# Performance work log

Measured on AMD Instinct MI355X. Metric: run time of the kernel, lower is better.

Reference implementation:

```python
import jax, jax.numpy as jnp
import numpy as np

BINS = 10
LOSS_WEIGHT = 1.0
EDGE_TOP = 1.0 + 1e-6  # edges[-1] += 1e-6 in the torch module


def setup_inputs() -> dict:
    key = jax.random.key(0)
    k1, k2, k3 = jax.random.split(key, 3)
    shape = (32, 1048576)
    # pred: sigmoid probabilities in [0, 1)
    pred = jax.random.uniform(k1, shape, dtype=jnp.float32)
    target = (jax.random.uniform(k2, shape) < 0.3).astype(jnp.float32)
    label_weight = (jax.random.uniform(k3, shape) < 0.95).astype(jnp.float32)
    return {"pred": pred, "target": target, "label_weight": label_weight}


def reference(pred, target, label_weight):
    p = pred.reshape(-1)
    t = target.reshape(-1).astype(p.dtype)
    lw = label_weight.reshape(-1).astype(p.dtype)

    I = jnp.sum(p * t)                       # intersection
    S = jnp.sum(p) + jnp.sum(t)              # denominator of Dice

    # gradient norm proxy: |2I/S * pred.detach() - target| (no grad flows through g)
    g = jax.lax.stop_gradient(jnp.abs(2.0 * I / S * p - t))

    valid = lw > 0
    tot = jnp.maximum(jnp.sum(valid.astype(p.dtype)), 1.0)

    # bin assignment: edges are i/bins for i=0..bins, with edges[-1] bumped by 1e-6,
    # so g in [i/bins, (i+1)/bins) -> bin i, and g in [1, 1+1e-6) -> bin bins-1.
    in_range = valid & (g < EDGE_TOP)
    bin_idx = jnp.clip(jnp.floor(g * BINS).astype(jnp.int32), 0, BINS - 1)

    # one-pass histogram of valid, in-range elements
    counts = jnp.zeros(BINS, dtype=p.dtype).at[bin_idx].add(in_range.astype(p.dtype))
    n_nonempty = jnp.sum(counts > 0).astype(p.dtype)

    # weight = tot / num_in_bin for elements in a non-empty bin, else 0; then /n
    per_elem = jnp.where(in_range, tot / jnp.maximum(counts[bin_idx], 1.0), 0.0)
    weights = per_elem / jnp.maximum(n_nonempty, 1.0)

    loss = 1.0 - jnp.sum(2.0 * p * t * weights) / S
    return loss * LOSS_WEIGHT
```

## Files before the change

### kernel.cpp

```cpp
#include <hip/hip_runtime.h>


constexpr int BINS = 10;
constexpr int K1   = 8;
constexpr int K2   = 8;
constexpr int CH1  = 256 * K1;
constexpr int CH2  = 256 * K2;
constexpr int OFF1 = 64;
constexpr int OFF2 = 16448;

__global__ __launch_bounds__(256) void k_reduce1(const float4* __restrict__ p,
                                                 const float4* __restrict__ t,
                                                 float* __restrict__ ws,
                                                 int n4, int n) {
    const int chunk = blockIdx.x * CH1;
    const int base  = chunk + threadIdx.x;
    float sI = 0.f, sP = 0.f, sT = 0.f;

    if (chunk + CH1 <= n4) {
        float4 pv[K1], tv[K1];
#pragma unroll
        for (int k = 0; k < K1; ++k) pv[k] = p[base + k * 256];
#pragma unroll
        for (int k = 0; k < K1; ++k) tv[k] = t[base + k * 256];
#pragma unroll
        for (int k = 0; k < K1; ++k) {
            sI += pv[k].x * tv[k].x + pv[k].y * tv[k].y + pv[k].z * tv[k].z + pv[k].w * tv[k].w;
            sP += pv[k].x + pv[k].y + pv[k].z + pv[k].w;
            sT += tv[k].x + tv[k].y + tv[k].z + tv[k].w;
        }
    } else {
        for (int k = 0; k < K1; ++k) {
            int i = base + k * 256;
            if (i < n4) {
                float4 pv = p[i], tv = t[i];
                sI += pv.x * tv.x + pv.y * tv.y + pv.z * tv.z + pv.w * tv.w;
                sP += pv.x + pv.y + pv.z + pv.w;
                sT += tv.x + tv.y + tv.z + tv.w;
            }
        }
    }
    if (blockIdx.x == 0 && threadIdx.x == 0) {
        const float* pf = (const float*)p;
        const float* tf = (const float*)t;
        for (int i = n4 * 4; i < n; ++i) { sI += pf[i] * tf[i]; sP += pf[i]; sT += tf[i]; }
    }
#pragma unroll
    for (int o = 32; o > 0; o >>= 1) {
        sI += __shfl_down(sI, o);
        sP += __shfl_down(sP, o);
        sT += __shfl_down(sT, o);
    }
    __shared__ float rI[4], rP[4], rT[4];
    int wave = threadIdx.x >> 6, lane = threadIdx.x & 63;
    if (lane == 0) { rI[wave] = sI; rP[wave] = sP; rT[wave] = sT; }
    __syncthreads();
    if (threadIdx.x == 0) {
        float* o = &ws[OFF1 + blockIdx.x * 4];
        o[0] = rI[0] + rI[1] + rI[2] + rI[3];
        o[1] = rP[0] + rP[1] + rP[2] + rP[3];
        o[2] = rT[0] + rT[1] + rT[2] + rT[3];
    }
}

__global__ __launch_bounds__(256) void k_mid(float* __restrict__ ws, int nb1) {
    const float4* pws = (const float4*)&ws[OFF1];
    float aI = 0.f, aP = 0.f, aT = 0.f;
    for (int b = threadIdx.x; b < nb1; b += 256) {
        float4 v = pws[b];
        aI += v.x; aP += v.y; aT += v.z;
    }
    __shared__ float red[256 * 5];
    float* mine = &red[threadIdx.x * 5];
    mine[0] = aI; mine[1] = aP; mine[2] = aT;
    __syncthreads();
    int tid = threadIdx.x;
    if (tid < 3) {
        float s = 0.f;
        for (int i = 0; i < 256; ++i) s += red[i * 5 + tid];
        red[tid] = s;
    }
    __syncthreads();
    if (tid == 0) {
        float I = red[0];
        float S = red[1] + red[2];
        ws[0] = 2.f * I / S;
        ws[1] = S;
    }
}

__global__ __launch_bounds__(256) void k_pass2(const float4* __restrict__ p,
                                               const float4* __restrict__ t,
                                               const float4* __restrict__ lw,
                                               float* __restrict__ ws,
                                               int n4, int n) {
    const float scale    = ws[0];
    const float edge_top = 1.0f + 1e-6f;

    float cnt[BINS], sm[BINS];
#pragma unroll
    for (int b = 0; b < BINS; ++b) { cnt[b] = 0.f; sm[b] = 0.f; }
    float vcount = 0.f;

    auto process = [&](float pe, float te, float we) {
        bool valid = we > 0.f;
        vcount += valid ? 1.f : 0.f;
        float g = fabsf(scale * pe - te);
        bool inr = valid && (g < edge_top);
        int b = (int)(g * 10.f);
        b = b > (BINS - 1) ? (BINS - 1) : b;
        float addc = inr ? 1.f : 0.f;
        float adds = inr ? 2.f * pe * te : 0.f;
#pragma unroll
        for (int b0 = 0; b0 < BINS; ++b0) {
            bool m = (b == b0);
            cnt[b0] += m ? addc : 0.f;
            sm[b0]  += m ? adds : 0.f;
        }
    };

    const int chunk = blockIdx.x * CH2;
    const int base  = chunk + threadIdx.x;

    if (chunk + CH2 <= n4) {
        float4 pv[K2], tv[K2], wv[K2];
#pragma unroll
        for (int k = 0; k < K2; ++k) pv[k] = p[base + k * 256];
#pragma unroll
        for (int k = 0; k < K2; ++k) tv[k] = t[base + k * 256];
#pragma unroll
        for (int k = 0; k < K2; ++k) wv[k] = lw[base + k * 256];
#pragma unroll
        for (int k = 0; k < K2; ++k) {
            process(pv[k].x, tv[k].x, wv[k].x);
            process(pv[k].y, tv[k].y, wv[k].y);
            process(pv[k].z, tv[k].z, wv[k].z);
            process(pv[k].w, tv[k].w, wv[k].w);
        }
    } else {
        for (int k = 0; k < K2; ++k) {
            int i = base + k * 256;
            if (i < n4) {
                float4 pv = p[i], tv = t[i], wv = lw[i];
                process(pv.x, tv.x, wv.x);
                process(pv.y, tv.y, wv.y);
                process(pv.z, tv.z, wv.z);
                process(pv.w, tv.w, wv.w);
            }
        }
    }
    if (blockIdx.x == 0 && threadIdx.x == 0) {
        const float* pf = (const float*)p;
        const float* tf = (const float*)t;
        const float* wf = (const float*)lw;
        for (int i = n4 * 4; i < n; ++i) process(pf[i], tf[i], wf[i]);
    }

    __shared__ float red[256 * 21];
    float* mine = &red[threadIdx.x * 21];
#pragma unroll
    for (int b0 = 0; b0 < BINS; ++b0) { mine[b0] = cnt[b0]; mine[BINS + b0] = sm[b0]; }
    mine[2 * BINS] = vcount;
    __syncthreads();

    int tid = threadIdx.x;
    if (tid < 2 * BINS + 1) {
        float v = 0.f;
        for (int i = 0; i < 256; ++i) v += red[i * 21 + tid];
        ws[OFF2 + blockIdx.x * 24 + tid] = v;
    }
}

__global__ __launch_bounds__(256) void k_final(const float* __restrict__ ws,
                                               float* __restrict__ out, int nb2) {
    float acc[24];
#pragma unroll
    for (int s = 0; s < 24; ++s) acc[s] = 0.f;

    for (int b = threadIdx.x; b < nb2; b += 256) {
        const float4* rec = (const float4*)&ws[OFF2 + b * 24];
        float4 v0 = rec[0], v1 = rec[1], v2 = rec[2],
               v3 = rec[3], v4 = rec[4], v5 = rec[5];
        acc[0]  += v0.x; acc[1]  += v0.y; acc[2]  += v0.z; acc[3]  += v0.w;
        acc[4]  += v1.x; acc[5]  += v1.y; acc[6]  += v1.z; acc[7]  += v1.w;
        acc[8]  += v2.x; acc[9]  += v2.y; acc[10] += v2.z; acc[11] += v2.w;
        acc[12] += v3.x; acc[13] += v3.y; acc[14] += v3.z; acc[15] += v3.w;
        acc[16] += v4.x; acc[17] += v4.y; acc[18] += v4.z; acc[19] += v4.w;
        acc[20] += v5.x;
    }

    __shared__ float red[256 * 25];
    float* mine = &red[threadIdx.x * 25];
#pragma unroll
    for (int s = 0; s <= 2 * BINS; ++s) mine[s] = acc[s];
    __syncthreads();

    __shared__ float fin[24];
    int tid = threadIdx.x;
    if (tid <= 2 * BINS) {
        float s = 0.f;
        for (int i = 0; i < 256; ++i) s += red[i * 25 + tid];
        fin[tid] = s;
    }
    __syncthreads();
    if (tid == 0) {
        float S   = ws[1];
        float tot = fmaxf(fin[20], 1.0f);
        int nne = 0;
        for (int b = 0; b < BINS; ++b) nne += (fin[b] > 0.f) ? 1 : 0;
        float nn = fmaxf((float)nne, 1.0f);
        float wsum = 0.f;
        for (int b = 0; b < BINS; ++b) {
            float c = fmaxf(fin[b], 1.0f);
            wsum += fin[BINS + b] * (tot / c);
        }
        wsum /= nn;
        out[0] = 1.0f - wsum / S;
    }
}

extern "C" void kernel_launch(void* const* d_in, const int* in_sizes, int n_in,
                              void* d_out, int out_size, void* d_ws, size_t ws_size,
                              hipStream_t stream) {
    const float* p  = (const float*)d_in[0];
    const float* t  = (const float*)d_in[1];
    const float* lw = (const float*)d_in[2];
    float* ws  = (float*)d_ws;
    float* out = (float*)d_out;
    int n  = in_sizes[0];
    int n4 = n >> 2;

    int nb1 = (n4 + CH1 - 1) / CH1;
    int nb2 = (n4 + CH2 - 1) / CH2;
    if (nb1 < 1) nb1 = 1;
    if (nb2 < 1) nb2 = 1;

    k_reduce1<<<nb1, 256, 0, stream>>>((const float4*)p, (const float4*)t, ws, n4, n);
    k_mid<<<1, 256, 0, stream>>>(ws, nb1);
    k_pass2<<<nb2, 256, 0, stream>>>((const float4*)p, (const float4*)t,
                                     (const float4*)lw, ws, n4, n);
    k_final<<<1, 256, 0, stream>>>(ws, out, nb2);
}
```

Measured before the change: 408.3 us.

## Use fixed-size grid-stride loops and integer bin counters in both reduction passes

```diff
diff --git a/kernel.cpp b/kernel.cpp
--- a/kernel.cpp
+++ b/kernel.cpp
@@ -1,49 +1,47 @@
 #include <hip/hip_runtime.h>
 
 
-constexpr int BINS = 10;
-constexpr int K1   = 8;
-constexpr int K2   = 8;
-constexpr int CH1  = 256 * K1;
-constexpr int CH2  = 256 * K2;
-constexpr int OFF1 = 64;
-constexpr int OFF2 = 16448;
+constexpr int BINS   = 10;
+constexpr int K      = 4;
+constexpr int CH     = 256 * K;
+constexpr int BLOCKS = 2048;
+constexpr int OFF1   = 64;
+constexpr int OFF2   = 16448;
 
 __global__ __launch_bounds__(256) void k_reduce1(const float4* __restrict__ p,
                                                  const float4* __restrict__ t,
                                                  float* __restrict__ ws,
                                                  int n4, int n) {
-    const int chunk = blockIdx.x * CH1;
-    const int base  = chunk + threadIdx.x;
+    const int tid   = threadIdx.x;
+    const int nfull = n4 / CH;
     float sI = 0.f, sP = 0.f, sT = 0.f;
 
-    if (chunk + CH1 <= n4) {
-        float4 pv[K1], tv[K1];
-#pragma unroll
-        for (int k = 0; k < K1; ++k) pv[k] = p[base + k * 256];
-#pragma unroll
-        for (int k = 0; k < K1; ++k) tv[k] = t[base + k * 256];
-#pragma unroll
-        for (int k = 0; k < K1; ++k) {
+    for (int c = blockIdx.x; c < nfull; c += gridDim.x) {
+        const int base = c * CH + tid;
+        float4 pv[K], tv[K];
+#pragma unroll
+        for (int k = 0; k < K; ++k) pv[k] = p[base + k * 256];
+#pragma unroll
+        for (int k = 0; k < K; ++k) tv[k] = t[base + k * 256];
+#pragma unroll
+        for (int k = 0; k < K; ++k) {
             sI += pv[k].x * tv[k].x + pv[k].y * tv[k].y + pv[k].z * tv[k].z + pv[k].w * tv[k].w;
             sP += pv[k].x + pv[k].y + pv[k].z + pv[k].w;
             sT += tv[k].x + tv[k].y + tv[k].z + tv[k].w;
         }
-    } else {
-        for (int k = 0; k < K1; ++k) {
-            int i = base + k * 256;
-            if (i < n4) {
-                float4 pv = p[i], tv = t[i];
-                sI += pv.x * tv.x + pv.y * tv.y + pv.z * tv.z + pv.w * tv.w;
-                sP += pv.x + pv.y + pv.z + pv.w;
-                sT += tv.x + tv.y + tv.z + tv.w;
-            }
-        }
-    }
-    if (blockIdx.x == 0 && threadIdx.x == 0) {
-        const float* pf = (const float*)p;
-        const float* tf = (const float*)t;
-        for (int i = n4 * 4; i < n; ++i) { sI += pf[i] * tf[i]; sP += pf[i]; sT += tf[i]; }
+    }
+    if (blockIdx.x == 0) {
+        for (int i = nfull * CH + tid; i < n4; i += 256) {
+            float4 pv = p[i], tv = t[i];
+            sI += pv.x * tv.x + pv.y * tv.y + pv.z * tv.z + pv.w * tv.w;
+            sP += pv.x + pv.y + pv.z + pv.w;
+            sT += tv.x + tv.y + tv.z + tv.w;
+        }
+        if (tid == 0) {
+            const float* pf = (const float*)p;
+            const float* tf = (const float*)t;
+            for (int i = n4 * 4; i < n; ++i) { sI += pf[i] * tf[i]; sP += pf[i]; sT += tf[i]; }
+        }
     }
 #pragma unroll
     for (int o = 32; o > 0; o >>= 1) {
@@ -52,10 +50,10 @@
         sT += __shfl_down(sT, o);
     }
     __shared__ float rI[4], rP[4], rT[4];
-    int wave = threadIdx.x >> 6, lane = threadIdx.x & 63;
+    int wave = tid >> 6, lane = tid & 63;
     if (lane == 0) { rI[wave] = sI; rP[wave] = sP; rT[wave] = sT; }
     __syncthreads();
-    if (threadIdx.x == 0) {
+    if (tid == 0) {
         float* o = &ws[OFF1 + blockIdx.x * 4];
         o[0] = rI[0] + rI[1] + rI[2] + rI[3];
         o[1] = rP[0] + rP[1] + rP[2] + rP[3];
@@ -96,74 +94,75 @@
                                                int n4, int n) {
     const float scale    = ws[0];
     const float edge_top = 1.0f + 1e-6f;
-
-    float cnt[BINS], sm[BINS];
-#pragma unroll
-    for (int b = 0; b < BINS; ++b) { cnt[b] = 0.f; sm[b] = 0.f; }
-    float vcount = 0.f;
+    const int tid   = threadIdx.x;
+    const int nfull = n4 / CH;
+
+    int   cnt[BINS];
+    float sm[BINS];
+#pragma unroll
+    for (int b = 0; b < BINS; ++b) { cnt[b] = 0; sm[b] = 0.f; }
+    int vcount = 0;
 
     auto process = [&](float pe, float te, float we) {
         bool valid = we > 0.f;
-        vcount += valid ? 1.f : 0.f;
+        vcount += valid;
         float g = fabsf(scale * pe - te);
         bool inr = valid && (g < edge_top);
         int b = (int)(g * 10.f);
         b = b > (BINS - 1) ? (BINS - 1) : b;
-        float addc = inr ? 1.f : 0.f;
-        float adds = inr ? 2.f * pe * te : 0.f;
+        int slot = inr ? b : BINS;
+        float adds = 2.f * pe * te;
 #pragma unroll
         for (int b0 = 0; b0 < BINS; ++b0) {
-            bool m = (b == b0);
-            cnt[b0] += m ? addc : 0.f;
+            bool m = (slot == b0);
+            cnt[b0] += m;
             sm[b0]  += m ? adds : 0.f;
         }
     };
 
-    const int chunk = blockIdx.x * CH2;
-    const int base  = chunk + threadIdx.x;
-
-    if (chunk + CH2 <= n4) {
-        float4 pv[K2], tv[K2], wv[K2];
-#pragma unroll
-        for (int k = 0; k < K2; ++k) pv[k] = p[base + k * 256];
-#pragma unroll
-        for (int k = 0; k < K2; ++k) tv[k] = t[base + k * 256];
-#pragma unroll
-        for (int k = 0; k < K2; ++k) wv[k] = lw[base + k * 256];
-#pragma unroll
-        for (int k = 0; k < K2; ++k) {
+    for (int c = blockIdx.x; c < nfull; c += gridDim.x) {
+        const int base = c * CH + tid;
+        float4 pv[K], tv[K], wv[K];
+#pragma unroll
+        for (int k = 0; k < K; ++k) pv[k] = p[base + k * 256];
+#pragma unroll
+        for (int k = 0; k < K; ++k) tv[k] = t[base + k * 256];
+#pragma unroll
+        for (int k = 0; k < K; ++k) wv[k] = lw[base + k * 256];
+#pragma unroll
+        for (int k = 0; k < K; ++k) {
             process(pv[k].x, tv[k].x, wv[k].x);
             process(pv[k].y, tv[k].y, wv[k].y);
             process(pv[k].z, tv[k].z, wv[k].z);
             process(pv[k].w, tv[k].w, wv[k].w);
         }
-    } else {
-        for (int k = 0; k < K2; ++k) {
-            int i = base + k * 256;
-            if (i < n4) {
-                float4 pv = p[i], tv = t[i], wv = lw[i];
-                process(pv.x, tv.x, wv.x);
-                process(pv.y, tv.y, wv.y);
-                process(pv.z, tv.z, wv.z);
-                process(pv.w, tv.w, wv.w);
-            }
-        }
-    }
-    if (blockIdx.x == 0 && threadIdx.x == 0) {
-        const float* pf = (const float*)p;
-        const float* tf = (const float*)t;
-        const float* wf = (const float*)lw;
-        for (int i = n4 * 4; i < n; ++i) process(pf[i], tf[i], wf[i]);
+    }
+    if (blockIdx.x == 0) {
+        for (int i = nfull * CH + tid; i < n4; i += 256) {
+            float4 pv = p[i], tv = t[i], wv = lw[i];
+            process(pv.x, tv.x, wv.x);
+            process(pv.y, tv.y, wv.y);
+            process(pv.z, tv.z, wv.z);
+            process(pv.w, tv.w, wv.w);
+        }
+        if (tid == 0) {
+            const float* pf = (const float*)p;
+            const float* tf = (const float*)t;
+            const float* wf = (const float*)lw;
+            for (int i = n4 * 4; i < n; ++i) process(pf[i], tf[i], wf[i]);
+        }
     }
 
     __shared__ float red[256 * 21];
-    float* mine = &red[threadIdx.x * 21];
-#pragma unroll
-    for (int b0 = 0; b0 < BINS; ++b0) { mine[b0] = cnt[b0]; mine[BINS + b0] = sm[b0]; }
-    mine[2 * BINS] = vcount;
-    __syncthreads();
-
-    int tid = threadIdx.x;
+    float* mine = &red[tid * 21];
+#pragma unroll
+    for (int b0 = 0; b0 < BINS; ++b0) {
+        mine[b0]        = (float)cnt[b0];
+        mine[BINS + b0] = sm[b0];
+    }
+    mine[2 * BINS] = (float)vcount;
+    __syncthreads();
+
     if (tid < 2 * BINS + 1) {
         float v = 0.f;
         for (int i = 0; i < 256; ++i) v += red[i * 21 + tid];
@@ -230,14 +229,9 @@
     int n  = in_sizes[0];
     int n4 = n >> 2;
 
-    int nb1 = (n4 + CH1 - 1) / CH1;
-    int nb2 = (n4 + CH2 - 1) / CH2;
-    if (nb1 < 1) nb1 = 1;
-    if (nb2 < 1) nb2 = 1;
-
-    k_reduce1<<<nb1, 256, 0, stream>>>((const float4*)p, (const float4*)t, ws, n4, n);
-    k_mid<<<1, 256, 0, stream>>>(ws, nb1);
-    k_pass2<<<nb2, 256, 0, stream>>>((const float4*)p, (const float4*)t,
-                                     (const float4*)lw, ws, n4, n);
-    k_final<<<1, 256, 0, stream>>>(ws, out, nb2);
-}
+    k_reduce1<<<BLOCKS, 256, 0, stream>>>((const float4*)p, (const float4*)t, ws, n4, n);
+    k_mid<<<1, 256, 0, stream>>>(ws, BLOCKS);
+    k_pass2<<<BLOCKS, 256, 0, stream>>>((const float4*)p, (const float4*)t,
+                                        (const float4*)lw, ws, n4, n);
+    k_final<<<1, 256, 0, stream>>>(ws, out, BLOCKS);
+}
```

Measured after the change: 401.3 us. No clear change (-1.7%).
